# Kernel tuning notes

Hardware: AMD Instinct MI355X
Metric: run time of the kernel (lower is better)

## Reference

```python
import jax, jax.numpy as jnp
import numpy as np

B, S, D, H, T = 64, 512, 1024, 1024, 9


def setup_inputs() -> dict:
    key = jax.random.key(0)
    ks = jax.random.split(key, 8)
    return {
        "input_": jax.random.normal(ks[0], (B, S, D), dtype=jnp.float32),
        "labels": jax.random.randint(ks[1], (B, S), 0, T),
        "attention_mask": jnp.ones((B, S), dtype=jnp.int32),
        # linear_1: input_dim -> hidden_dim (stored [in, out])
        "W1": (jax.random.normal(ks[2], (D, H), dtype=jnp.float32) * 0.02),
        "b1": jnp.zeros((H,), dtype=jnp.float32),
        # linear_2: hidden_dim -> tag_dim
        "W2": (jax.random.normal(ks[3], (H, T), dtype=jnp.float32) * 0.02),
        "b2": jnp.zeros((T,), dtype=jnp.float32),
        # torchcrf params: uniform(-0.1, 0.1)
        "start_trans": jax.random.uniform(ks[4], (T,), minval=-0.1, maxval=0.1),
        "end_trans": jax.random.uniform(ks[5], (T,), minval=-0.1, maxval=0.1),
        "trans": jax.random.uniform(ks[6], (T, T), minval=-0.1, maxval=0.1),
    }


def _crf_mean_llh(logits, tags, mask, start, end, trans):
    """torchcrf.CRF log-likelihood, reduction='mean'. logits [B,S,T]."""
    nb = logits.shape[0]
    em = jnp.transpose(logits, (1, 0, 2))          # [S,B,T] time-major
    tg = tags.T                                    # [S,B]
    m = mask.T.astype(logits.dtype)                # [S,B]
    bidx = jnp.arange(nb)

    # --- numerator: score of the gold path ---
    score0 = start[tg[0]] + em[0, bidx, tg[0]]

    def num_step(carry, x):
        score, last = carry
        em_t, tag_t, m_t = x
        score = score + (trans[last, tag_t] + em_t[bidx, tag_t]) * m_t
        last = jnp.where(m_t > 0, tag_t, last)
        return (score, last), None

    (score, last), _ = jax.lax.scan(num_step, (score0, tg[0]), (em[1:], tg[1:], m[1:]))
    score = score + end[last]

    # --- denominator: log-partition via logsumexp forward recurrence ---
    alpha0 = start[None, :] + em[0]                # [B,T]

    def part_step(alpha, x):
        em_t, m_t = x
        # [B, prev T, next T] semiring (log-sum-exp) matrix product
        nxt = jax.nn.logsumexp(alpha[:, :, None] + trans[None, :, :] + em_t[:, None, :], axis=1)
        alpha = jnp.where(m_t[:, None] > 0, nxt, alpha)
        return alpha, None

    alpha, _ = jax.lax.scan(part_step, alpha0, (em[1:], m[1:]))
    log_z = jax.nn.logsumexp(alpha + end[None, :], axis=1)

    return jnp.mean(score - log_z)


def reference(input_, labels, attention_mask, W1, b1, W2, b2, start_trans, end_trans, trans):
    # dropout layers are identity in eval mode
    h = input_ @ W1 + b1                           # [B,S,H]
    logits = h @ W2 + b2                           # [B,S,T]
    llh = _crf_mean_llh(logits, labels, attention_mask, start_trans, end_trans, trans)
    loss = -llh                                    # forward returns (-1*crf_llh, logits)
    return (loss, logits)
```

## Files before the change

### kernel.cpp

```cpp
#include <hip/hip_runtime.h>

#define BD 64
#define SD 512
#define DD 1024
#define HD 1024
#define TD 9
#define NSEG 16
#define SEGL 32
#define NEGI -1e30f

__device__ __forceinline__ float lse9(const float v[9]) {
    float m0 = fmaxf(v[0], v[1]);
    float m1 = fmaxf(v[2], v[3]);
    float m2 = fmaxf(v[4], v[5]);
    float m3 = fmaxf(v[6], v[7]);
    float mx = fmaxf(fmaxf(m0, m1), fmaxf(fmaxf(m2, m3), v[8]));
    float s = __expf(v[0] - mx) + __expf(v[1] - mx) + __expf(v[2] - mx)
            + __expf(v[3] - mx) + __expf(v[4] - mx) + __expf(v[5] - mx)
            + __expf(v[6] - mx) + __expf(v[7] - mx) + __expf(v[8] - mx);
    return mx + __logf(s);
}

__global__ __launch_bounds__(256) void k_w12(const float* __restrict__ W1,
                                             const float* __restrict__ b1,
                                             const float* __restrict__ W2,
                                             const float* __restrict__ b2,
                                             float* __restrict__ W12t,
                                             float* __restrict__ b12) {
    __shared__ float sh_w2[HD * TD];
    __shared__ float wred[4][TD];
    const int tid = threadIdx.x;
    const int wave = tid >> 6, lane = tid & 63;
    const int d = blockIdx.x;

    for (int i = tid; i < HD * TD / 4; i += 256)
        ((float4*)sh_w2)[i] = ((const float4*)W2)[i];
    __syncthreads();

    const float* row = (d < DD) ? (W1 + (size_t)d * HD) : b1;
    float4 x = ((const float4*)row)[tid];

    float acc[TD];
#pragma unroll
    for (int t = 0; t < TD; t++) acc[t] = 0.f;
#pragma unroll
    for (int u = 0; u < 4; u++) {
        float xv = (&x.x)[u];
        int h = tid * 4 + u;
#pragma unroll
        for (int t = 0; t < TD; t++) acc[t] += xv * sh_w2[h * TD + t];
    }
#pragma unroll
    for (int t = 0; t < TD; t++) {
        float v = acc[t];
#pragma unroll
        for (int m = 1; m < 64; m <<= 1) v += __shfl_xor(v, m);
        acc[t] = v;
    }
    if (lane == 0) {
#pragma unroll
        for (int t = 0; t < TD; t++) wred[wave][t] = acc[t];
    }
    __syncthreads();
    if (tid < TD) {
        float s = wred[0][tid] + wred[1][tid] + wred[2][tid] + wred[3][tid];
        if (d < DD) W12t[tid * DD + d] = s;
        else        b12[tid] = s + b2[tid];
    }
}

__global__ __launch_bounds__(256) void k_gemm2(const float* __restrict__ X,
                                               const float* __restrict__ W12t,
                                               const float* __restrict__ b12,
                                               float* __restrict__ logits) {
    __shared__ float wt[TD][DD];
    __shared__ float bb[TD];

    for (int i = threadIdx.x; i < TD * DD / 4; i += 256)
        ((float4*)&wt[0][0])[i] = ((const float4*)W12t)[i];
    if (threadIdx.x < TD) bb[threadIdx.x] = b12[threadIdx.x];
    __syncthreads();

    const int wave = threadIdx.x >> 6;
    const int lane = threadIdx.x & 63;
    const int g = lane >> 4;
    const int l16 = lane & 15;
    const int row0 = blockIdx.x * 32 + wave * 8 + g * 2;

    const float4* xr0 = (const float4*)(X + (size_t)row0 * DD);
    const float4* xr1 = xr0 + DD / 4;

    float acc0[TD], acc1[TD];
#pragma unroll
    for (int t = 0; t < TD; t++) { acc0[t] = 0.f; acc1[t] = 0.f; }

#pragma unroll 4
    for (int k = 0; k < 16; k++) {
        int d4 = l16 + k * 16;
        float4 x0 = xr0[d4];
        float4 x1 = xr1[d4];
#pragma unroll
        for (int t = 0; t < TD; t++) {
            const float4 w = *(const float4*)&wt[t][d4 * 4];
            acc0[t] += x0.x * w.x + x0.y * w.y + x0.z * w.z + x0.w * w.w;
            acc1[t] += x1.x * w.x + x1.y * w.y + x1.z * w.z + x1.w * w.w;
        }
    }

#pragma unroll
    for (int t = 0; t < TD; t++) {
        float v0 = acc0[t], v1 = acc1[t];
        v0 += __shfl_xor(v0, 1); v1 += __shfl_xor(v1, 1);
        v0 += __shfl_xor(v0, 2); v1 += __shfl_xor(v1, 2);
        v0 += __shfl_xor(v0, 4); v1 += __shfl_xor(v1, 4);
        v0 += __shfl_xor(v0, 8); v1 += __shfl_xor(v1, 8);
        acc0[t] = v0; acc1[t] = v1;
    }

    float* out0 = logits + (size_t)row0 * TD;
    float* out1 = out0 + TD;
    if (l16 < TD) {
        out0[l16] = acc0[l16] + bb[l16];
        out1[l16] = acc1[l16] + bb[l16];
    }
}

__global__ __launch_bounds__(256) void k_crf_seg(const float* __restrict__ logits,
                                                 const int* __restrict__ maskp,
                                                 const float* __restrict__ transp,
                                                 float* __restrict__ segP) {
    const int blk = blockIdx.x;
    const int b = blk >> 4, s = blk & 15;
    const int tid = threadIdx.x;

    __shared__ float tr[81];
    __shared__ float em[SEGL * 9];
    __shared__ int   mk[SEGL];
    __shared__ float bufA[16 * 81];
    __shared__ float bufB[8 * 81];

    const int t0 = s * SEGL + 1;

    {
        const float* src = logits + ((size_t)b * SD + t0) * TD;
        for (int i = tid; i < SEGL * 9; i += 256)
            em[i] = (t0 + i / 9 < SD) ? src[i] : 0.f;
    }
    if (tid < SEGL) {
        int t = t0 + tid;
        mk[tid] = (t < SD) ? maskp[b * SD + t] : 0;
    }
    if (tid < 81) tr[tid] = transp[tid];
    __syncthreads();

    for (int e = tid; e < 16 * 81; e += 256) {
        int p = e / 81, r = e - p * 81;
        int i = r / 9, j = r - i * 9;
        int la = 2 * p, lb = 2 * p + 1;
        int mA = mk[la], mB = mk[lb];
        float o;
        if (mA && mB) {
            float v[9];
#pragma unroll
            for (int k = 0; k < 9; k++)
                v[k] = tr[i * 9 + k] + em[la * 9 + k] + tr[k * 9 + j];
            o = lse9(v) + em[lb * 9 + j];
        } else if (mA) {
            o = tr[r] + em[la * 9 + j];
        } else if (mB) {
            o = tr[r] + em[lb * 9 + j];
        } else {
            o = (i == j) ? 0.f : NEGI;
        }
        bufA[e] = o;
    }
    __syncthreads();

#define COMBINE(SRC, DST, NP)                                        \
    for (int e = tid; e < (NP) * 81; e += 256) {                     \
        int p = e / 81, r = e - p * 81;                              \
        int i = r / 9, j = r - i * 9;                                \
        const float* Am = (SRC) + (2 * p) * 81;                      \
        const float* Bm = Am + 81;                                   \
        float v[9];                                                  \
        _Pragma("unroll")                                            \
        for (int k = 0; k < 9; k++) v[k] = Am[i * 9 + k] + Bm[k * 9 + j]; \
        (DST)[e] = lse9(v);                                          \
    }                                                                \
    __syncthreads();

    COMBINE(bufA, bufB, 8)
    COMBINE(bufB, bufA, 4)
    COMBINE(bufA, bufB, 2)

    if (tid < 81) {
        int i = tid / 9, j = tid - (tid / 9) * 9;
        float v[9];
#pragma unroll
        for (int k = 0; k < 9; k++) v[k] = bufB[i * 9 + k] + bufB[81 + k * 9 + j];
        segP[(size_t)blk * 81 + tid] = lse9(v);
    }
}

__global__ __launch_bounds__(256) void k_crf_fin(const float* __restrict__ logits,
                                                 const int* __restrict__ labels,
                                                 const int* __restrict__ maskp,
                                                 const float* __restrict__ startp,
                                                 const float* __restrict__ endp,
                                                 const float* __restrict__ transp,
                                                 const float* __restrict__ segP,
                                                 float* __restrict__ diff) {
    const int b = blockIdx.x;
    const int tid = threadIdx.x;

    __shared__ float S[16 * 81];
    __shared__ float A8[8 * 81];
    __shared__ float A4[4 * 81];
    __shared__ float A2[2 * 81];
    __shared__ float P[81];
    __shared__ float finv[81];
    __shared__ float red[256];
    __shared__ int   redi[256];

    for (int i = tid; i < 16 * 81; i += 256) S[i] = segP[(size_t)b * NSEG * 81 + i];
    __syncthreads();

    COMBINE(S, A8, 8)
    COMBINE(A8, A4, 4)
    COMBINE(A4, A2, 2)

    if (tid < 81) {
        int i = tid / 9, j = tid - (tid / 9) * 9;
        float v[9];
#pragma unroll
        for (int k = 0; k < 9; k++) v[k] = A2[i * 9 + k] + A2[81 + k * 9 + j];
        P[tid] = lse9(v);
    }
    __syncthreads();

    if (tid < 81) {
        int k = tid / 9, j = tid - (tid / 9) * 9;
        finv[tid] = startp[k] + logits[(size_t)b * SD * TD + k] + P[tid] + endp[j];
    }

    float part = 0.f;
    for (int t = 1 + tid; t < SD; t += 256) {
        if (maskp[b * SD + t]) {
            int tgp = labels[b * SD + t - 1];
            int tgc = labels[b * SD + t];
            part += transp[tgp * TD + tgc] + logits[((size_t)b * SD + t) * TD + tgc];
        }
    }
    int lastt = 0;
    for (int t = tid; t < SD; t += 256) {
        if (maskp[b * SD + t]) lastt = max(lastt, t);
    }
    red[tid] = part;
    redi[tid] = lastt;
    __syncthreads();

    if (tid < 64) {
        float p4 = red[tid] + red[tid + 64] + red[tid + 128] + red[tid + 192];
        int l4 = max(max(redi[tid], redi[tid + 64]), max(redi[tid + 128], redi[tid + 192]));
#pragma unroll
        for (int m = 1; m < 64; m <<= 1) {
            p4 += __shfl_xor(p4, m);
            l4 = max(l4, __shfl_xor(l4, m));
        }
        float v1 = finv[tid];
        float v2 = (tid + 64 < 81) ? finv[tid + 64] : NEGI;
        float mx = fmaxf(v1, v2);
#pragma unroll
        for (int m = 1; m < 64; m <<= 1) mx = fmaxf(mx, __shfl_xor(mx, m));
        float ssum = __expf(v1 - mx) + __expf(v2 - mx);
#pragma unroll
        for (int m = 1; m < 64; m <<= 1) ssum += __shfl_xor(ssum, m);
        float logz = mx + __logf(ssum);

        if (tid == 0) {
            int tg0 = labels[b * SD];
            int tgl = labels[b * SD + l4];
            float score = p4 + startp[tg0] + logits[(size_t)b * SD * TD + tg0] + endp[tgl];
            diff[b] = score - logz;
        }
    }
}

__global__ __launch_bounds__(64) void k_loss(const float* __restrict__ diff,
                                             float* __restrict__ out) {
    float v = (threadIdx.x < BD) ? diff[threadIdx.x] : 0.f;
#pragma unroll
    for (int m = 1; m < 64; m <<= 1) v += __shfl_xor(v, m);
    if (threadIdx.x == 0) out[0] = -v / (float)BD;
}

extern "C" void kernel_launch(void* const* d_in, const int* in_sizes, int n_in,
                              void* d_out, int out_size, void* d_ws, size_t ws_size,
                              hipStream_t stream) {
    const float* X      = (const float*)d_in[0];
    const int*   labels = (const int*)d_in[1];
    const int*   maskp  = (const int*)d_in[2];
    const float* W1     = (const float*)d_in[3];
    const float* b1     = (const float*)d_in[4];
    const float* W2     = (const float*)d_in[5];
    const float* b2     = (const float*)d_in[6];
    const float* startp = (const float*)d_in[7];
    const float* endp   = (const float*)d_in[8];
    const float* transp = (const float*)d_in[9];

    float* out = (float*)d_out;
    float* ws = (float*)d_ws;

    float* diff = ws;
    float* W12t = ws + 64;
    float* b12  = ws + 64 + DD * TD;
    float* segP = ws + 64 + DD * TD + 16;
    float* logits = out + 1;

    hipLaunchKernelGGL(k_w12, dim3(DD + 1), dim3(256), 0, stream,
                       W1, b1, W2, b2, W12t, b12);
    hipLaunchKernelGGL(k_gemm2, dim3(BD * SD / 32), dim3(256), 0, stream,
                       X, W12t, b12, logits);
    hipLaunchKernelGGL(k_crf_seg, dim3(BD * NSEG), dim3(256), 0, stream,
                       logits, maskp, transp, segP);
    hipLaunchKernelGGL(k_crf_fin, dim3(BD), dim3(256), 0, stream,
                       logits, labels, maskp, startp, endp, transp, segP, diff);
    hipLaunchKernelGGL(k_loss, dim3(1), dim3(64), 0, stream, diff, out);
}
```

Baseline: 60.02 us.

## Fuse logits GEMV with CRF segment scan and drop separate loss kernel

```diff
diff --git a/kernel.cpp b/kernel.cpp
--- a/kernel.cpp
+++ b/kernel.cpp
@@ -26,30 +26,28 @@
                                              const float* __restrict__ W2,
                                              const float* __restrict__ b2,
                                              float* __restrict__ W12t,
-                                             float* __restrict__ b12) {
-    __shared__ float sh_w2[HD * TD];
+                                             float* __restrict__ b12,
+                                             float* __restrict__ out) {
     __shared__ float wred[4][TD];
     const int tid = threadIdx.x;
     const int wave = tid >> 6, lane = tid & 63;
     const int d = blockIdx.x;
 
-    for (int i = tid; i < HD * TD / 4; i += 256)
-        ((float4*)sh_w2)[i] = ((const float4*)W2)[i];
-    __syncthreads();
+    if (d == 0 && tid == 0) out[0] = 0.f;
 
     const float* row = (d < DD) ? (W1 + (size_t)d * HD) : b1;
     float4 x = ((const float4*)row)[tid];
 
+    float w[36];
+    const float4* wp = (const float4*)(W2 + (size_t)tid * 36);
+#pragma unroll
+    for (int u = 0; u < 9; u++) ((float4*)w)[u] = wp[u];
+
     float acc[TD];
 #pragma unroll
-    for (int t = 0; t < TD; t++) acc[t] = 0.f;
-#pragma unroll
-    for (int u = 0; u < 4; u++) {
-        float xv = (&x.x)[u];
-        int h = tid * 4 + u;
-#pragma unroll
-        for (int t = 0; t < TD; t++) acc[t] += xv * sh_w2[h * TD + t];
-    }
+    for (int t = 0; t < TD; t++)
+        acc[t] = x.x * w[t] + x.y * w[9 + t] + x.z * w[18 + t] + x.w * w[27 + t];
+
 #pragma unroll
     for (int t = 0; t < TD; t++) {
         float v = acc[t];
@@ -69,25 +67,39 @@
     }
 }
 
-__global__ __launch_bounds__(256) void k_gemm2(const float* __restrict__ X,
-                                               const float* __restrict__ W12t,
-                                               const float* __restrict__ b12,
-                                               float* __restrict__ logits) {
-    __shared__ float wt[TD][DD];
+__global__ __launch_bounds__(256) void k_gemm_seg(const float* __restrict__ X,
+                                                  const float* __restrict__ W12t,
+                                                  const float* __restrict__ b12,
+                                                  const int* __restrict__ maskp,
+                                                  const float* __restrict__ transp,
+                                                  float* __restrict__ logits,
+                                                  float* __restrict__ segP) {
+    __shared__ float smem[TD * DD];
+    __shared__ float em[SEGL * TD];
+    __shared__ int   mk[SEGL];
+    __shared__ float tr[81];
     __shared__ float bb[TD];
 
-    for (int i = threadIdx.x; i < TD * DD / 4; i += 256)
-        ((float4*)&wt[0][0])[i] = ((const float4*)W12t)[i];
-    if (threadIdx.x < TD) bb[threadIdx.x] = b12[threadIdx.x];
-    __syncthreads();
-
-    const int wave = threadIdx.x >> 6;
-    const int lane = threadIdx.x & 63;
-    const int g = lane >> 4;
-    const int l16 = lane & 15;
-    const int row0 = blockIdx.x * 32 + wave * 8 + g * 2;
-
-    const float4* xr0 = (const float4*)(X + (size_t)row0 * DD);
+    const int blk = blockIdx.x;
+    const int b = blk >> 4, s = blk & 15;
+    const int tid = threadIdx.x;
+    const int wave = tid >> 6, lane = tid & 63;
+    const int g = lane >> 4, l16 = lane & 15;
+    const int grp = wave * 4 + g;
+    const int t0 = s * SEGL;
+
+    for (int i = tid; i < TD * DD / 4; i += 256)
+        ((float4*)smem)[i] = ((const float4*)W12t)[i];
+    if (tid < TD) bb[tid] = b12[tid];
+    if (tid < 81) tr[tid] = transp[tid];
+    if (tid < SEGL) {
+        int t = t0 + 1 + tid;
+        mk[tid] = (t < SD) ? maskp[b * SD + t] : 0;
+    }
+    __syncthreads();
+
+    const int row0 = t0 + grp * 2;
+    const float4* xr0 = (const float4*)(X + ((size_t)b * SD + row0) * DD);
     const float4* xr1 = xr0 + DD / 4;
 
     float acc0[TD], acc1[TD];
@@ -101,7 +113,7 @@
         float4 x1 = xr1[d4];
 #pragma unroll
         for (int t = 0; t < TD; t++) {
-            const float4 w = *(const float4*)&wt[t][d4 * 4];
+            const float4 w = *(const float4*)&smem[t * DD + d4 * 4];
             acc0[t] += x0.x * w.x + x0.y * w.y + x0.z * w.z + x0.w * w.w;
             acc1[t] += x1.x * w.x + x1.y * w.y + x1.z * w.z + x1.w * w.w;
         }
@@ -117,41 +129,46 @@
         acc0[t] = v0; acc1[t] = v1;
     }
 
-    float* out0 = logits + (size_t)row0 * TD;
-    float* out1 = out0 + TD;
     if (l16 < TD) {
-        out0[l16] = acc0[l16] + bb[l16];
-        out1[l16] = acc1[l16] + bb[l16];
-    }
-}
-
-__global__ __launch_bounds__(256) void k_crf_seg(const float* __restrict__ logits,
-                                                 const int* __restrict__ maskp,
-                                                 const float* __restrict__ transp,
-                                                 float* __restrict__ segP) {
-    const int blk = blockIdx.x;
-    const int b = blk >> 4, s = blk & 15;
-    const int tid = threadIdx.x;
-
-    __shared__ float tr[81];
-    __shared__ float em[SEGL * 9];
-    __shared__ int   mk[SEGL];
-    __shared__ float bufA[16 * 81];
-    __shared__ float bufB[8 * 81];
-
-    const int t0 = s * SEGL + 1;
-
-    {
-        const float* src = logits + ((size_t)b * SD + t0) * TD;
-        for (int i = tid; i < SEGL * 9; i += 256)
-            em[i] = (t0 + i / 9 < SD) ? src[i] : 0.f;
-    }
-    if (tid < SEGL) {
-        int t = t0 + tid;
-        mk[tid] = (t < SD) ? maskp[b * SD + t] : 0;
-    }
-    if (tid < 81) tr[tid] = transp[tid];
-    __syncthreads();
+        float v0 = acc0[l16] + bb[l16];
+        float v1 = acc1[l16] + bb[l16];
+        float* o = logits + ((size_t)b * SD + row0) * TD;
+        o[l16] = v0;
+        o[TD + l16] = v1;
+        if (grp > 0) em[(grp * 2 - 1) * TD + l16] = v0;
+        em[(grp * 2) * TD + l16] = v1;
+    }
+
+    if (s < NSEG - 1) {
+        const float4* xrb = (const float4*)(X + ((size_t)b * SD + t0 + SEGL) * DD);
+        float accb[TD];
+#pragma unroll
+        for (int t = 0; t < TD; t++) accb[t] = 0.f;
+#pragma unroll 4
+        for (int k = 0; k < 16; k++) {
+            int d4 = l16 + k * 16;
+            float4 xb = xrb[d4];
+#pragma unroll
+            for (int t = 0; t < TD; t++) {
+                const float4 w = *(const float4*)&smem[t * DD + d4 * 4];
+                accb[t] += xb.x * w.x + xb.y * w.y + xb.z * w.z + xb.w * w.w;
+            }
+        }
+#pragma unroll
+        for (int t = 0; t < TD; t++) {
+            float v = accb[t];
+            v += __shfl_xor(v, 1);
+            v += __shfl_xor(v, 2);
+            v += __shfl_xor(v, 4);
+            v += __shfl_xor(v, 8);
+            accb[t] = v;
+        }
+        if (tid < TD) em[(SEGL - 1) * TD + tid] = accb[tid] + bb[tid];
+    }
+    __syncthreads();
+
+    float* bufA = smem;
+    float* bufB = smem + 16 * 81;
 
     for (int e = tid; e < 16 * 81; e += 256) {
         int p = e / 81, r = e - p * 81;
@@ -209,7 +226,7 @@
                                                  const float* __restrict__ endp,
                                                  const float* __restrict__ transp,
                                                  const float* __restrict__ segP,
-                                                 float* __restrict__ diff) {
+                                                 float* __restrict__ out) {
     const int b = blockIdx.x;
     const int tid = threadIdx.x;
 
@@ -281,17 +298,9 @@
             int tg0 = labels[b * SD];
             int tgl = labels[b * SD + l4];
             float score = p4 + startp[tg0] + logits[(size_t)b * SD * TD + tg0] + endp[tgl];
-            diff[b] = score - logz;
-        }
-    }
-}
-
-__global__ __launch_bounds__(64) void k_loss(const float* __restrict__ diff,
-                                             float* __restrict__ out) {
-    float v = (threadIdx.x < BD) ? diff[threadIdx.x] : 0.f;
-#pragma unroll
-    for (int m = 1; m < 64; m <<= 1) v += __shfl_xor(v, m);
-    if (threadIdx.x == 0) out[0] = -v / (float)BD;
+            atomicAdd(out, -(score - logz) / (float)BD);
+        }
+    }
 }
 
 extern "C" void kernel_launch(void* const* d_in, const int* in_sizes, int n_in,
@@ -311,19 +320,15 @@
     float* out = (float*)d_out;
     float* ws = (float*)d_ws;
 
-    float* diff = ws;
     float* W12t = ws + 64;
     float* b12  = ws + 64 + DD * TD;
     float* segP = ws + 64 + DD * TD + 16;
     float* logits = out + 1;
 
     hipLaunchKernelGGL(k_w12, dim3(DD + 1), dim3(256), 0, stream,
-                       W1, b1, W2, b2, W12t, b12);
-    hipLaunchKernelGGL(k_gemm2, dim3(BD * SD / 32), dim3(256), 0, stream,
-                       X, W12t, b12, logits);
-    hipLaunchKernelGGL(k_crf_seg, dim3(BD * NSEG), dim3(256), 0, stream,
-                       logits, maskp, transp, segP);
+                       W1, b1, W2, b2, W12t, b12, out);
+    hipLaunchKernelGGL(k_gemm_seg, dim3(BD * NSEG), dim3(256), 0, stream,
+                       X, W12t, b12, maskp, transp, logits, segP);
     hipLaunchKernelGGL(k_crf_fin, dim3(BD), dim3(256), 0, stream,
-                       logits, labels, maskp, startp, endp, transp, segP, diff);
-    hipLaunchKernelGGL(k_loss, dim3(1), dim3(64), 0, stream, diff, out);
-}
+                       logits, labels, maskp, startp, endp, transp, segP, out);
+}
```

Result: slower. 63.08 us (+5.1%).

## Split-K the logits GEMV with atomics, drop W2 smem staging and loss kernel

Applied to the files above, without the earlier changes.

```diff
diff --git a/kernel.cpp b/kernel.cpp
--- a/kernel.cpp
+++ b/kernel.cpp
@@ -7,6 +7,7 @@
 #define TD 9
 #define NSEG 16
 #define SEGL 32
+#define HK 128
 #define NEGI -1e30f
 
 __device__ __forceinline__ float lse9(const float v[9]) {
@@ -26,30 +27,36 @@
                                              const float* __restrict__ W2,
                                              const float* __restrict__ b2,
                                              float* __restrict__ W12t,
-                                             float* __restrict__ b12) {
-    __shared__ float sh_w2[HD * TD];
+                                             float* __restrict__ b12,
+                                             float* __restrict__ logits,
+                                             float* __restrict__ out) {
     __shared__ float wred[4][TD];
     const int tid = threadIdx.x;
     const int wave = tid >> 6, lane = tid & 63;
     const int d = blockIdx.x;
 
-    for (int i = tid; i < HD * TD / 4; i += 256)
-        ((float4*)sh_w2)[i] = ((const float4*)W2)[i];
-    __syncthreads();
+    if (d == 0 && tid == 0) out[0] = 0.f;
+    {
+        int base = d * 288;
+        for (int i = tid; i < 288; i += 256) {
+            int idx = base + i;
+            if (idx < BD * SD * TD) logits[idx] = 0.f;
+        }
+    }
 
     const float* row = (d < DD) ? (W1 + (size_t)d * HD) : b1;
     float4 x = ((const float4*)row)[tid];
 
+    float w[36];
+    const float4* wp = (const float4*)(W2 + (size_t)tid * 36);
+#pragma unroll
+    for (int u = 0; u < 9; u++) ((float4*)w)[u] = wp[u];
+
     float acc[TD];
 #pragma unroll
-    for (int t = 0; t < TD; t++) acc[t] = 0.f;
-#pragma unroll
-    for (int u = 0; u < 4; u++) {
-        float xv = (&x.x)[u];
-        int h = tid * 4 + u;
-#pragma unroll
-        for (int t = 0; t < TD; t++) acc[t] += xv * sh_w2[h * TD + t];
-    }
+    for (int t = 0; t < TD; t++)
+        acc[t] = x.x * w[t] + x.y * w[9 + t] + x.z * w[18 + t] + x.w * w[27 + t];
+
 #pragma unroll
     for (int t = 0; t < TD; t++) {
         float v = acc[t];
@@ -69,25 +76,29 @@
     }
 }
 
-__global__ __launch_bounds__(256) void k_gemm2(const float* __restrict__ X,
-                                               const float* __restrict__ W12t,
-                                               const float* __restrict__ b12,
-                                               float* __restrict__ logits) {
-    __shared__ float wt[TD][DD];
+__global__ __launch_bounds__(256) void k_gemm2h(const float* __restrict__ X,
+                                                const float* __restrict__ W12t,
+                                                const float* __restrict__ b12,
+                                                float* __restrict__ logits) {
+    __shared__ float wt[TD][HK * 4];
     __shared__ float bb[TD];
 
-    for (int i = threadIdx.x; i < TD * DD / 4; i += 256)
-        ((float4*)&wt[0][0])[i] = ((const float4*)W12t)[i];
-    if (threadIdx.x < TD) bb[threadIdx.x] = b12[threadIdx.x];
-    __syncthreads();
-
-    const int wave = threadIdx.x >> 6;
-    const int lane = threadIdx.x & 63;
-    const int g = lane >> 4;
-    const int l16 = lane & 15;
-    const int row0 = blockIdx.x * 32 + wave * 8 + g * 2;
-
-    const float4* xr0 = (const float4*)(X + (size_t)row0 * DD);
+    const int blk = blockIdx.x;
+    const int h = blk & 1, rowgrp = blk >> 1;
+    const int tid = threadIdx.x;
+
+    for (int i = tid; i < TD * HK; i += 256) {
+        int t = i >> 7, d4 = i & (HK - 1);
+        ((float4*)&wt[t][0])[d4] = ((const float4*)W12t)[t * 256 + h * HK + d4];
+    }
+    if (tid < TD) bb[tid] = b12[tid];
+    __syncthreads();
+
+    const int wave = tid >> 6, lane = tid & 63;
+    const int g = lane >> 4, l16 = lane & 15;
+    const int row0 = rowgrp * 32 + wave * 8 + g * 2;
+
+    const float4* xr0 = (const float4*)(X + (size_t)row0 * DD) + h * HK;
     const float4* xr1 = xr0 + DD / 4;
 
     float acc0[TD], acc1[TD];
@@ -95,7 +106,7 @@
     for (int t = 0; t < TD; t++) { acc0[t] = 0.f; acc1[t] = 0.f; }
 
 #pragma unroll 4
-    for (int k = 0; k < 16; k++) {
+    for (int k = 0; k < 8; k++) {
         int d4 = l16 + k * 16;
         float4 x0 = xr0[d4];
         float4 x1 = xr1[d4];
@@ -117,11 +128,12 @@
         acc0[t] = v0; acc1[t] = v1;
     }
 
-    float* out0 = logits + (size_t)row0 * TD;
-    float* out1 = out0 + TD;
     if (l16 < TD) {
-        out0[l16] = acc0[l16] + bb[l16];
-        out1[l16] = acc1[l16] + bb[l16];
+        float a0 = acc0[l16] + (h ? 0.f : bb[l16]);
+        float a1 = acc1[l16] + (h ? 0.f : bb[l16]);
+        float* o = logits + (size_t)row0 * TD;
+        atomicAdd(&o[l16], a0);
+        atomicAdd(&o[TD + l16], a1);
     }
 }
 
@@ -209,7 +221,7 @@
                                                  const float* __restrict__ endp,
                                                  const float* __restrict__ transp,
                                                  const float* __restrict__ segP,
-                                                 float* __restrict__ diff) {
+                                                 float* __restrict__ out) {
     const int b = blockIdx.x;
     const int tid = threadIdx.x;
 
@@ -281,17 +293,9 @@
             int tg0 = labels[b * SD];
             int tgl = labels[b * SD + l4];
             float score = p4 + startp[tg0] + logits[(size_t)b * SD * TD + tg0] + endp[tgl];
-            diff[b] = score - logz;
-        }
-    }
-}
-
-__global__ __launch_bounds__(64) void k_loss(const float* __restrict__ diff,
-                                             float* __restrict__ out) {
-    float v = (threadIdx.x < BD) ? diff[threadIdx.x] : 0.f;
-#pragma unroll
-    for (int m = 1; m < 64; m <<= 1) v += __shfl_xor(v, m);
-    if (threadIdx.x == 0) out[0] = -v / (float)BD;
+            atomicAdd(out, -(score - logz) / (float)BD);
+        }
+    }
 }
 
 extern "C" void kernel_launch(void* const* d_in, const int* in_sizes, int n_in,
@@ -311,19 +315,17 @@
     float* out = (float*)d_out;
     float* ws = (float*)d_ws;
 
-    float* diff = ws;
     float* W12t = ws + 64;
     float* b12  = ws + 64 + DD * TD;
     float* segP = ws + 64 + DD * TD + 16;
     float* logits = out + 1;
 
     hipLaunchKernelGGL(k_w12, dim3(DD + 1), dim3(256), 0, stream,
-                       W1, b1, W2, b2, W12t, b12);
-    hipLaunchKernelGGL(k_gemm2, dim3(BD * SD / 32), dim3(256), 0, stream,
+                       W1, b1, W2, b2, W12t, b12, logits, out);
+    hipLaunchKernelGGL(k_gemm2h, dim3(BD * SD / 32 * 2), dim3(256), 0, stream,
                        X, W12t, b12, logits);
     hipLaunchKernelGGL(k_crf_seg, dim3(BD * NSEG), dim3(256), 0, stream,
                        logits, maskp, transp, segP);
     hipLaunchKernelGGL(k_crf_fin, dim3(BD), dim3(256), 0, stream,
-                       logits, labels, maskp, startp, endp, transp, segP, diff);
-    hipLaunchKernelGGL(k_loss, dim3(1), dim3(64), 0, stream, diff, out);
-}
+                       logits, labels, maskp, startp, endp, transp, segP, out);
+}
```

Measured after the change: 60.87 us. No clear change (+1.4%).
